# Optimization experiments

Hardware: AMD Instinct MI355X
Metric: run time of the kernel (lower is better)

## Reference

```python
import jax, jax.numpy as jnp
import numpy as np

DIM = 2048
N_HEADS = 32
N_KV_HEADS = 8
HEAD_DIM = DIM // N_HEADS  # 64
N_REP = N_HEADS // N_KV_HEADS  # 4
B, S = 1, 2048


def _rope(t, cos, sin):
    # t: (b, s, h, head_dim); cos/sin: (s, head_dim//2)
    tr = t.reshape(*t.shape[:-1], -1, 2)
    a, b = tr[..., 0], tr[..., 1]
    c = cos[None, :, None, :]
    s_ = sin[None, :, None, :]
    ra = a * c - b * s_
    rb = a * s_ + b * c
    return jnp.stack([ra, rb], axis=-1).reshape(t.shape)


def setup_inputs() -> dict:
    key = jax.random.key(0)
    ks = jax.random.split(key, 6)
    sc = 1.0 / np.sqrt(DIM)
    x = jax.random.normal(ks[0], (B, S, DIM), dtype=jnp.float32)
    wq = jax.random.normal(ks[1], (DIM, N_HEADS * HEAD_DIM), dtype=jnp.float32) * sc
    wk = jax.random.normal(ks[2], (DIM, N_KV_HEADS * HEAD_DIM), dtype=jnp.float32) * sc
    wv = jax.random.normal(ks[3], (DIM, N_KV_HEADS * HEAD_DIM), dtype=jnp.float32) * sc
    wo = jax.random.normal(ks[4], (N_HEADS * HEAD_DIM, DIM), dtype=jnp.float32) * sc
    # rotary frequencies (theta = 500000 as in Llama3)
    inv = 1.0 / (500000.0 ** (np.arange(0, HEAD_DIM, 2, dtype=np.float32) / HEAD_DIM))
    ang = np.arange(S, dtype=np.float32)[:, None] * inv[None, :]
    freqs_cos = jnp.asarray(np.cos(ang), dtype=jnp.float32)
    freqs_sin = jnp.asarray(np.sin(ang), dtype=jnp.float32)
    # causal additive mask
    mask = jnp.triu(jnp.full((S, S), -1e9, dtype=jnp.float32), k=1)
    return {"x": x, "wq": wq, "wk": wk, "wv": wv, "wo": wo,
            "freqs_cos": freqs_cos, "freqs_sin": freqs_sin, "mask": mask,
            "start_pos": 0}


def reference(x, wq, wk, wv, wo, freqs_cos, freqs_sin, mask, start_pos):
    b, s, _ = x.shape
    xq = (x @ wq).reshape(b, s, N_HEADS, HEAD_DIM)
    xk = (x @ wk).reshape(b, s, N_KV_HEADS, HEAD_DIM)
    xv = (x @ wv).reshape(b, s, N_KV_HEADS, HEAD_DIM)
    xq = _rope(xq, freqs_cos, freqs_sin)
    xk = _rope(xk, freqs_cos, freqs_sin)
    # GQA without repeat_interleave: view queries as (b, s, kv, rep, d)
    q = xq.reshape(b, s, N_KV_HEADS, N_REP, HEAD_DIM)
    scale = 1.0 / np.sqrt(HEAD_DIM)
    # scores: (b, kv, rep, q, k)
    scores = jnp.einsum('bqkrd,bskd->bkrqs', q, xk) * scale
    scores = scores + mask[None, None, None, :, :]
    probs = jax.nn.softmax(scores.astype(jnp.float32), axis=-1).astype(x.dtype)
    out = jnp.einsum('bkrqs,bskd->bqkrd', probs, xv)
    out = out.reshape(b, s, N_HEADS * HEAD_DIM)
    return out @ wo
```

## Files before the change

kernel.cpp:

```cpp
#include <hip/hip_runtime.h>
#include <hip/hip_bf16.h>

#define DIM 2048
#define S_LEN 2048
#define N_HEADS 32
#define N_KV_HEADS 8
#define HEAD_DIM 64
#define KV_DIM (N_KV_HEADS * HEAD_DIM)
#define QKV_N (DIM + 2 * KV_DIM)
#define QSCALE 0.18033688011112042f

typedef __attribute__((ext_vector_type(8))) short bf16x8;
typedef __attribute__((ext_vector_type(4))) float f32x4;

__device__ __forceinline__ unsigned short bf16_of(float f) {
    __hip_bfloat16 h = __float2bfloat16(f);
    return *reinterpret_cast<unsigned short*>(&h);
}
__device__ __forceinline__ float f_of_bf16(unsigned short u) {
    unsigned int x = ((unsigned int)u) << 16;
    return __uint_as_float(x);
}
__device__ __forceinline__ void gl_lds16(const void* g, void* l) {
    __builtin_amdgcn_global_load_lds((const __attribute__((address_space(1))) void*)g,
                                     (__attribute__((address_space(3))) void*)l, 16, 0, 0);
}
__device__ __forceinline__ unsigned int pack2tr(float lo, float hi) {
    return __builtin_amdgcn_perm(__float_as_uint(hi), __float_as_uint(lo), 0x07060302u);
}
__device__ __forceinline__ float max3f(float a, float b, float c) {
    float d;
    asm("v_max3_f32 %0, %1, %2, %3" : "=v"(d) : "v"(a), "v"(b), "v"(c));
    return d;
}

__global__ __launch_bounds__(256) void prep(const float* __restrict__ x,
                                            const float* __restrict__ wq,
                                            const float* __restrict__ wk,
                                            const float* __restrict__ wv,
                                            const float* __restrict__ wo,
                                            unsigned short* __restrict__ xbf,
                                            unsigned short* __restrict__ wqkvT,
                                            unsigned short* __restrict__ woT) {
    __shared__ float tile[64][65];
    const int t = threadIdx.x;
    int b = blockIdx.x;
    if (b < 4096) {
        int idx = b * 256 + t;
        float4 f = ((const float4*)x)[idx];
        ushort4 u;
        u.x = bf16_of(f.x); u.y = bf16_of(f.y); u.z = bf16_of(f.z); u.w = bf16_of(f.w);
        ((ushort4*)xbf)[idx] = u;
        return;
    }
    b -= 4096;
    const float* src;
    unsigned short* dst;
    int src_cols, bx, by;
    if (b < 1024)      { src = wq; dst = wqkvT;                                src_cols = DIM;    bx = b & 31;          by = b >> 5; }
    else if (b < 1280) { src = wk; dst = wqkvT + (size_t)DIM * DIM;            src_cols = KV_DIM; bx = (b - 1024) & 7;  by = (b - 1024) >> 3; }
    else if (b < 1536) { src = wv; dst = wqkvT + (size_t)(DIM + KV_DIM) * DIM; src_cols = KV_DIM; bx = (b - 1280) & 7;  by = (b - 1280) >> 3; }
    else               { src = wo; dst = woT;                                  src_cols = DIM;    bx = (b - 1536) & 31; by = (b - 1536) >> 5; }
    const int c0 = bx * 64, r0 = by * 64;
#pragma unroll
    for (int i = 0; i < 16; i++) {
        int idx = t + i * 256;
        int r = idx >> 6, c = idx & 63;
        tile[r][c] = src[(size_t)(r0 + r) * src_cols + c0 + c];
    }
    __syncthreads();
#pragma unroll
    for (int i = 0; i < 8; i++) {
        int idx = t + i * 256;
        int rr = idx >> 5, cc = (idx & 31) * 2;
        ushort2 u2;
        u2.x = bf16_of(tile[cc][rr]);
        u2.y = bf16_of(tile[cc + 1][rr]);
        *(ushort2*)&dst[(size_t)(c0 + rr) * DIM + r0 + cc] = u2;
    }
}

__global__ __launch_bounds__(256) void gemm_bt64(const unsigned short* __restrict__ A,
                                                 const unsigned short* __restrict__ Bt,
                                                 void* __restrict__ Cv,
                                                 int M, int N, int K, int c_bf16) {
    __shared__ unsigned short As[3][128 * 64];
    __shared__ unsigned short Bs[3][64 * 64];
    const int tid = threadIdx.x;
    const int wave = tid >> 6, lane = tid & 63;
    const int m16 = lane & 15, quad = lane >> 4;
    const int m0 = blockIdx.y * 128, n0 = blockIdx.x * 64;
    const int wm = (wave >> 1) * 64, wn = (wave & 1) * 32;

    const int lrow = lane >> 3;
    const int gc = (lane & 7) ^ lrow;
    const unsigned short* Ab = A + (size_t)(m0 + wave * 8 + lrow) * K + gc * 8;
    const unsigned short* Bb = Bt + (size_t)(n0 + wave * 8 + lrow) * K + gc * 8;

    f32x4 acc[4][2];
#pragma unroll
    for (int mb = 0; mb < 4; mb++)
#pragma unroll
        for (int nb = 0; nb < 2; nb++) acc[mb][nb] = (f32x4){0.f, 0.f, 0.f, 0.f};

    auto STAGE = [&](int t, int bufi) {
        const int k0 = t << 6;
#pragma unroll
        for (int g = 0; g < 4; g++)
            gl_lds16(Ab + (size_t)g * 32 * K + k0, &As[bufi][(g * 32 + wave * 8) * 64]);
#pragma unroll
        for (int g = 0; g < 2; g++)
            gl_lds16(Bb + (size_t)g * 32 * K + k0, &Bs[bufi][(g * 32 + wave * 8) * 64]);
    };

    STAGE(0, 0);
    STAGE(1, 1);

    const int nt = K >> 6;
    for (int kt = 0; kt < nt; kt++) {
        if (kt + 1 < nt) asm volatile("s_waitcnt vmcnt(6)" ::: "memory");
        else             asm volatile("s_waitcnt vmcnt(0)" ::: "memory");
        __builtin_amdgcn_s_barrier();
        __builtin_amdgcn_sched_barrier(0);
        if (kt + 2 < nt) STAGE(kt + 2, (kt + 2) % 3);

        const unsigned short* A_ = As[kt % 3];
        const unsigned short* B_ = Bs[kt % 3];
#pragma unroll
        for (int ks = 0; ks < 2; ks++) {
            const int ch = (ks * 4 + quad) ^ (m16 & 7);
            bf16x8 af[4], bfr[2];
#pragma unroll
            for (int mb = 0; mb < 4; mb++)
                af[mb] = *(const bf16x8*)&A_[(wm + mb * 16 + m16) * 64 + ch * 8];
#pragma unroll
            for (int nb = 0; nb < 2; nb++)
                bfr[nb] = *(const bf16x8*)&B_[(wn + nb * 16 + m16) * 64 + ch * 8];
#pragma unroll
            for (int mb = 0; mb < 4; mb++)
#pragma unroll
                for (int nb = 0; nb < 2; nb++)
                    acc[mb][nb] = __builtin_amdgcn_mfma_f32_16x16x32_bf16(af[mb], bfr[nb], acc[mb][nb], 0, 0, 0);
        }
    }

    if (c_bf16) {
        unsigned short* C = (unsigned short*)Cv;
#pragma unroll
        for (int mb = 0; mb < 4; mb++)
#pragma unroll
            for (int nb = 0; nb < 2; nb++)
#pragma unroll
                for (int r = 0; r < 4; r++)
                    C[(size_t)(m0 + wm + mb * 16 + quad * 4 + r) * N + n0 + wn + nb * 16 + m16] =
                        bf16_of(acc[mb][nb][r]);
    } else {
        float* C = (float*)Cv;
#pragma unroll
        for (int mb = 0; mb < 4; mb++)
#pragma unroll
            for (int nb = 0; nb < 2; nb++)
#pragma unroll
                for (int r = 0; r < 4; r++)
                    C[(size_t)(m0 + wm + mb * 16 + quad * 4 + r) * N + n0 + wn + nb * 16 + m16] =
                        acc[mb][nb][r];
    }
}

__global__ __launch_bounds__(256) void rope_kv(const unsigned short* __restrict__ qkv,
                                               unsigned short* __restrict__ kbf,
                                               unsigned short* __restrict__ vbt,
                                               const float* __restrict__ fcos,
                                               const float* __restrict__ fsin) {
    __shared__ unsigned short tile[64][65];
    const int t = threadIdx.x;
    int b = blockIdx.x;
    if (b < 512) {
        int idx = b * 256 + t;
        int s = idx >> 6;
        int rem = idx & 63;
        int hh = rem >> 3, j = rem & 7;
        int srcoff = s * QKV_N + DIM + hh * 64 + j * 8;
        int dstoff = s * KV_DIM + hh * 64 + j * 8;
        bf16x8 v8 = *(const bf16x8*)&qkv[srcoff];
        float4 c4 = *(const float4*)&fcos[s * 32 + j * 4];
        float4 s4 = *(const float4*)&fsin[s * 32 + j * 4];
        float cs[4] = {c4.x, c4.y, c4.z, c4.w};
        float sn[4] = {s4.x, s4.y, s4.z, s4.w};
        bf16x8 o;
#pragma unroll
        for (int p = 0; p < 4; p++) {
            float a = f_of_bf16((unsigned short)v8[2 * p]);
            float bb = f_of_bf16((unsigned short)v8[2 * p + 1]);
            o[2 * p]     = (short)bf16_of(a * cs[p] - bb * sn[p]);
            o[2 * p + 1] = (short)bf16_of(a * sn[p] + bb * cs[p]);
        }
        *(bf16x8*)&kbf[dstoff] = o;
        return;
    }
    b -= 512;
    const int d0 = (b & 7) * 64;
    const int s0 = (b >> 3) * 64;
#pragma unroll
    for (int i = 0; i < 16; i++) {
        int idx = t + i * 256;
        int r = idx >> 6, c = idx & 63;
        tile[r][c] = qkv[(size_t)(s0 + r) * QKV_N + DIM + KV_DIM + d0 + c];
    }
    __syncthreads();
#pragma unroll
    for (int i = 0; i < 16; i++) {
        int idx = t + i * 256;
        int r = idx >> 6, c = idx & 63;
        int key = s0 + c;
        int kl = key & 127;
        int kp = (kl & 0x60) | ((kl & 0x0C) << 1) | ((kl & 0x10) >> 2) | (kl & 3);
        vbt[(size_t)(d0 + r) * S_LEN + (key & ~127) + kp] = tile[c][r];
    }
}

__global__ __launch_bounds__(256) void attn_mfma9(const unsigned short* __restrict__ qkv,
                                                  const unsigned short* __restrict__ kb,
                                                  const unsigned short* __restrict__ vbt,
                                                  const float* __restrict__ fcos,
                                                  const float* __restrict__ fsin,
                                                  unsigned short* __restrict__ out) {
    const int h  = blockIdx.x;
    const int qt = 31 - (int)blockIdx.y;
    const int kh = h >> 2;
    const int tid  = threadIdx.x;
    const int wave = tid >> 6;
    const int lane = tid & 63;
    const int m16  = lane & 15;
    const int quad = lane >> 4;

    __shared__ unsigned short Ks[2][128 * 64];
    __shared__ unsigned short Vt[64 * 128];

    const int lrow8 = lane >> 3;
    const int kc    = (lane & 7) ^ lrow8;
    const int lrow4 = lane >> 4;
    const int vc    = (lane & 15) ^ ((wave * 4 + lrow4) & 7);

    const unsigned short* Kbase = kb + (size_t)kh * 64 + (size_t)(wave * 8 + lrow8) * KV_DIM + kc * 8;
    const unsigned short* Vbase = vbt + (size_t)(kh * 64 + wave * 4 + lrow4) * S_LEN + vc * 8;

    bf16x8 ones;
#pragma unroll
    for (int i = 0; i < 8; i++) ones[i] = (short)0x3F80;

    const int q0 = qt * 64;
    const int n_iter = (qt >> 1) + 1;

    bf16x8 qa[2];
    {
        const int qrow = q0 + wave * 16 + m16;
        const unsigned short* qsrc = qkv + (size_t)qrow * QKV_N + h * 64;
#pragma unroll
        for (int ks = 0; ks < 2; ks++) {
            bf16x8 raw = *(const bf16x8*)&qsrc[ks * 32 + quad * 8];
            float4 c4 = *(const float4*)&fcos[qrow * 32 + ks * 16 + quad * 4];
            float4 s4 = *(const float4*)&fsin[qrow * 32 + ks * 16 + quad * 4];
            float cs[4] = {c4.x, c4.y, c4.z, c4.w};
            float sn[4] = {s4.x, s4.y, s4.z, s4.w};
#pragma unroll
            for (int p = 0; p < 4; p++) {
                float a = f_of_bf16((unsigned short)raw[2 * p]);
                float bb = f_of_bf16((unsigned short)raw[2 * p + 1]);
                qa[ks][2 * p]     = (short)bf16_of((a * cs[p] - bb * sn[p]) * QSCALE);
                qa[ks][2 * p + 1] = (short)bf16_of((a * sn[p] + bb * cs[p]) * QSCALE);
            }
        }
    }

    f32x4 o_acc[4];
#pragma unroll
    for (int nb = 0; nb < 4; nb++) o_acc[nb] = (f32x4){0.f, 0.f, 0.f, 0.f};
    f32x4 l_acc = (f32x4){0.f, 0.f, 0.f, 0.f};
    float m_s = -1e30f;
    const int qrow_lane = q0 + wave * 16 + m16;
    const int orow_base = q0 + wave * 16 + quad * 4;

#pragma unroll
    for (int g = 0; g < 4; g++)
        gl_lds16(Kbase + (size_t)(g * 32) * KV_DIM, &Ks[0][(g * 32 + wave * 8) * 64]);

    for (int kt = 0; kt < n_iter; kt++) {
        asm volatile("s_waitcnt vmcnt(0)" ::: "memory");
        __builtin_amdgcn_s_barrier();
        __builtin_amdgcn_sched_barrier(0);

        const int knext = (kt + 1 < n_iter) ? (kt + 1) : kt;
#pragma unroll
        for (int g = 0; g < 4; g++)
            gl_lds16(Vbase + (size_t)g * 16 * S_LEN + kt * 128,
                     &Vt[(g * 16 + wave * 4) * 128]);
#pragma unroll
        for (int g = 0; g < 4; g++)
            gl_lds16(Kbase + (size_t)(knext * 128 + g * 32) * KV_DIM,
                     &Ks[(kt + 1) & 1][(g * 32 + wave * 8) * 64]);

        const unsigned short* K_ = Ks[kt & 1];

        f32x4 sc[8];
#pragma unroll
        for (int cb = 0; cb < 8; cb++) sc[cb] = (f32x4){0.f, 0.f, 0.f, 0.f};
        __builtin_amdgcn_s_setprio(1);
#pragma unroll
        for (int ks = 0; ks < 2; ks++) {
            const int slot = (ks * 4 + quad) ^ (m16 & 7);
#pragma unroll
            for (int cb = 0; cb < 8; cb++) {
                bf16x8 kf = *(const bf16x8*)&K_[(cb * 16 + m16) * 64 + slot * 8];
                sc[cb] = __builtin_amdgcn_mfma_f32_16x16x32_bf16(kf, qa[ks], sc[cb], 0, 0, 0);
            }
        }
        __builtin_amdgcn_s_setprio(0);

        if (kt == n_iter - 1) {
#pragma unroll
            for (int cb = 0; cb < 8; cb++) {
                int key = kt * 128 + cb * 16 + quad * 4;
#pragma unroll
                for (int r = 0; r < 4; r++)
                    if (key + r > qrow_lane) sc[cb][r] = -1e30f;
            }
        }

        float rmax = fmaxf(sc[0][0], sc[0][1]);
        rmax = max3f(sc[0][2], sc[0][3], rmax);
#pragma unroll
        for (int cb = 1; cb < 8; cb++) {
            rmax = max3f(sc[cb][0], sc[cb][1], rmax);
            rmax = max3f(sc[cb][2], sc[cb][3], rmax);
        }
        rmax = fmaxf(rmax, __shfl_xor(rmax, 16, 64));
        rmax = fmaxf(rmax, __shfl_xor(rmax, 32, 64));

        if (!__all(rmax - m_s <= 8.0f)) {
            float mnew = fmaxf(m_s, rmax);
            float alpha = __builtin_amdgcn_exp2f(m_s - mnew);
            m_s = mnew;
#pragma unroll
            for (int r = 0; r < 4; r++) {
                float a_r = __shfl(alpha, quad * 4 + r, 64);
#pragma unroll
                for (int nb = 0; nb < 4; nb++) o_acc[nb][r] *= a_r;
                l_acc[r] *= a_r;
            }
        }

#pragma unroll
        for (int cb = 0; cb < 8; cb++)
#pragma unroll
            for (int r = 0; r < 4; r++)
                sc[cb][r] = __builtin_amdgcn_exp2f(sc[cb][r] - m_s);

        unsigned int P01[8], P23[8];
#pragma unroll
        for (int cb = 0; cb < 8; cb++) {
            P01[cb] = pack2tr(sc[cb][0], sc[cb][1]);
            P23[cb] = pack2tr(sc[cb][2], sc[cb][3]);
        }

        asm volatile("s_waitcnt vmcnt(4)" ::: "memory");
        __builtin_amdgcn_s_barrier();
        __builtin_amdgcn_sched_barrier(0);

        __builtin_amdgcn_s_setprio(1);
#pragma unroll
        for (int ks = 0; ks < 4; ks++) {
            union { unsigned int u[4]; bf16x8 v; } pa;
            pa.u[0] = P01[2 * ks];     pa.u[1] = P23[2 * ks];
            pa.u[2] = P01[2 * ks + 1]; pa.u[3] = P23[2 * ks + 1];
            const int slot = (ks * 4 + quad) ^ (m16 & 7);
#pragma unroll
            for (int nb = 0; nb < 4; nb++) {
                bf16x8 vf = *(const bf16x8*)&Vt[(nb * 16 + m16) * 128 + slot * 8];
                o_acc[nb] = __builtin_amdgcn_mfma_f32_16x16x32_bf16(pa.v, vf, o_acc[nb], 0, 0, 0);
            }
            l_acc = __builtin_amdgcn_mfma_f32_16x16x32_bf16(pa.v, ones, l_acc, 0, 0, 0);
        }
        __builtin_amdgcn_s_setprio(0);
    }

#pragma unroll
    for (int r = 0; r < 4; r++) {
        float inv_l = 1.f / l_acc[r];
#pragma unroll
        for (int nb = 0; nb < 4; nb++)
            out[(size_t)(orow_base + r) * DIM + h * 64 + nb * 16 + m16] =
                bf16_of(o_acc[nb][r] * inv_l);
    }
}

extern "C" void kernel_launch(void* const* d_in, const int* in_sizes, int n_in,
                              void* d_out, int out_size, void* d_ws, size_t ws_size,
                              hipStream_t stream) {
    const float* x    = (const float*)d_in[0];
    const float* wq   = (const float*)d_in[1];
    const float* wk   = (const float*)d_in[2];
    const float* wv   = (const float*)d_in[3];
    const float* wo   = (const float*)d_in[4];
    const float* fcos = (const float*)d_in[5];
    const float* fsin = (const float*)d_in[6];

    char* ws = (char*)d_ws;
    const size_t MB = 1024 * 1024;
    unsigned short* xbf    = (unsigned short*)(ws);
    unsigned short* wqkvT  = (unsigned short*)(ws + 8 * MB);
    unsigned short* woT    = (unsigned short*)(ws + 20 * MB);
    unsigned short* qkvbf  = (unsigned short*)(ws + 28 * MB);
    unsigned short* vbt    = (unsigned short*)(ws + 40 * MB);
    unsigned short* kbf    = (unsigned short*)(ws + 16 * MB);
    unsigned short* attnbf = (unsigned short*)(ws);

    prep<<<4096 + 2560, 256, 0, stream>>>(x, wq, wk, wv, wo, xbf, wqkvT, woT);

    gemm_bt64<<<dim3(QKV_N / 64, S_LEN / 128), 256, 0, stream>>>(xbf, wqkvT, qkvbf,
                                                                 S_LEN, QKV_N, DIM, 1);

    rope_kv<<<512 + 256, 256, 0, stream>>>(qkvbf, kbf, vbt, fcos, fsin);

    attn_mfma9<<<dim3(N_HEADS, 32), 256, 0, stream>>>(qkvbf, kbf, vbt, fcos, fsin, attnbf);

    gemm_bt64<<<dim3(DIM / 64, S_LEN / 128), 256, 0, stream>>>(attnbf, woT, d_out,
                                                               S_LEN, DIM, DIM, 0);
}
```

Baseline: 239.3 us.

## Vectorize weight transpose loads and switch GEMM to two-stage LDS buffering

The weight transpose/convert kernel now reads float4 vectors from global memory and writes ushort4 bf16 values, replacing scalar loads and ushort2 stores. This is meant to cut memory instruction count in the per-call weight preparation. The GEMM drops from a three-buffer global_load_lds pipeline with explicit vmcnt waits to a two-buffer scheme synchronized by __syncthreads. That lowers LDS use per block and may allow more resident blocks, but the prefetch depth shrinks to one tile, so load latency is hidden less.

```diff
diff --git a/kernel.cpp b/kernel.cpp
--- a/kernel.cpp
+++ b/kernel.cpp
@@ -63,20 +63,24 @@
     else               { src = wo; dst = woT;                                  src_cols = DIM;    bx = (b - 1536) & 31; by = (b - 1536) >> 5; }
     const int c0 = bx * 64, r0 = by * 64;
 #pragma unroll
-    for (int i = 0; i < 16; i++) {
+    for (int i = 0; i < 4; i++) {
         int idx = t + i * 256;
-        int r = idx >> 6, c = idx & 63;
-        tile[r][c] = src[(size_t)(r0 + r) * src_cols + c0 + c];
+        int r = idx >> 4, c4 = (idx & 15) * 4;
+        float4 f = *(const float4*)&src[(size_t)(r0 + r) * src_cols + c0 + c4];
+        tile[r][c4 + 0] = f.x; tile[r][c4 + 1] = f.y;
+        tile[r][c4 + 2] = f.z; tile[r][c4 + 3] = f.w;
     }
     __syncthreads();
 #pragma unroll
-    for (int i = 0; i < 8; i++) {
+    for (int i = 0; i < 4; i++) {
         int idx = t + i * 256;
-        int rr = idx >> 5, cc = (idx & 31) * 2;
-        ushort2 u2;
-        u2.x = bf16_of(tile[cc][rr]);
-        u2.y = bf16_of(tile[cc + 1][rr]);
-        *(ushort2*)&dst[(size_t)(c0 + rr) * DIM + r0 + cc] = u2;
+        int rr = idx >> 4, cc = (idx & 15) * 4;
+        ushort4 u;
+        u.x = bf16_of(tile[cc + 0][rr]);
+        u.y = bf16_of(tile[cc + 1][rr]);
+        u.z = bf16_of(tile[cc + 2][rr]);
+        u.w = bf16_of(tile[cc + 3][rr]);
+        *(ushort4*)&dst[(size_t)(c0 + rr) * DIM + r0 + cc] = u;
     }
 }
 
@@ -84,8 +88,8 @@
                                                  const unsigned short* __restrict__ Bt,
                                                  void* __restrict__ Cv,
                                                  int M, int N, int K, int c_bf16) {
-    __shared__ unsigned short As[3][128 * 64];
-    __shared__ unsigned short Bs[3][64 * 64];
+    __shared__ unsigned short As[2][128 * 64];
+    __shared__ unsigned short Bs[2][64 * 64];
     const int tid = threadIdx.x;
     const int wave = tid >> 6, lane = tid & 63;
     const int m16 = lane & 15, quad = lane >> 4;
@@ -103,29 +107,28 @@
 #pragma unroll
         for (int nb = 0; nb < 2; nb++) acc[mb][nb] = (f32x4){0.f, 0.f, 0.f, 0.f};
 
-    auto STAGE = [&](int t, int bufi) {
-        const int k0 = t << 6;
-#pragma unroll
-        for (int g = 0; g < 4; g++)
-            gl_lds16(Ab + (size_t)g * 32 * K + k0, &As[bufi][(g * 32 + wave * 8) * 64]);
-#pragma unroll
-        for (int g = 0; g < 2; g++)
-            gl_lds16(Bb + (size_t)g * 32 * K + k0, &Bs[bufi][(g * 32 + wave * 8) * 64]);
-    };
-
-    STAGE(0, 0);
-    STAGE(1, 1);
+#pragma unroll
+    for (int g = 0; g < 4; g++)
+        gl_lds16(Ab + (size_t)g * 32 * K, &As[0][(g * 32 + wave * 8) * 64]);
+#pragma unroll
+    for (int g = 0; g < 2; g++)
+        gl_lds16(Bb + (size_t)g * 32 * K, &Bs[0][(g * 32 + wave * 8) * 64]);
 
     const int nt = K >> 6;
     for (int kt = 0; kt < nt; kt++) {
-        if (kt + 1 < nt) asm volatile("s_waitcnt vmcnt(6)" ::: "memory");
-        else             asm volatile("s_waitcnt vmcnt(0)" ::: "memory");
-        __builtin_amdgcn_s_barrier();
-        __builtin_amdgcn_sched_barrier(0);
-        if (kt + 2 < nt) STAGE(kt + 2, (kt + 2) % 3);
-
-        const unsigned short* A_ = As[kt % 3];
-        const unsigned short* B_ = Bs[kt % 3];
+        __syncthreads();
+        if (kt + 1 < nt) {
+            const int nb2 = (kt + 1) & 1;
+            const int k0 = (kt + 1) << 6;
+#pragma unroll
+            for (int g = 0; g < 4; g++)
+                gl_lds16(Ab + (size_t)g * 32 * K + k0, &As[nb2][(g * 32 + wave * 8) * 64]);
+#pragma unroll
+            for (int g = 0; g < 2; g++)
+                gl_lds16(Bb + (size_t)g * 32 * K + k0, &Bs[nb2][(g * 32 + wave * 8) * 64]);
+        }
+        const unsigned short* A_ = As[kt & 1];
+        const unsigned short* B_ = Bs[kt & 1];
 #pragma unroll
         for (int ks = 0; ks < 2; ks++) {
             const int ch = (ks * 4 + quad) ^ (m16 & 7);
```

Measured after the change: 215.9 us. 1.11x faster.
